# Kernel optimization log

Hardware: AMD Instinct MI355X
Metric: run time of the kernel (lower is better)

## Reference

```python
import jax, jax.numpy as jnp
import numpy as np

SR = 16000
MIN_W = 2.0 * np.pi * 20.0 / SR   # from TimeVaryingLPBiquad(min_w=2*pi*20/sr)
MAX_W = float(np.pi)
MIN_Q = 0.5
MAX_Q = 2.0                        # max_q init arg
MIN_D = 0.1
MAX_D = 2.0

B, T = 32, 65536


def map_logspace(sig, lo, hi):
    # exp-interpolation between lo and hi: lo * (hi/lo)**sig
    return lo * jnp.power(hi / lo, sig)


def setup_inputs() -> dict:
    key = jax.random.key(0)
    k1, k2, k3, k4 = jax.random.split(key, 4)
    f0 = 40.0 + 360.0 * jax.random.uniform(k1, (B, T), dtype=jnp.float32)  # period in samples
    x = jax.random.normal(k2, (B, T), dtype=jnp.float32)
    params = jax.random.normal(k3, (B, T, 4), dtype=jnp.float32)
    onsets = (jax.random.uniform(k4, (B, T)) < 5e-4).astype(jnp.int32)
    return {"f0": f0, "input": x, "params": params, "onsets": onsets}


def _average_per_onset(params, onsets):
    # segment ids = cumulative count of onsets; average params within each segment
    Bb, Tt, C = params.shape
    seg = jnp.cumsum(onsets, axis=1)                       # [B,T] ints in [0, T]
    flat = (jnp.arange(Bb, dtype=seg.dtype)[:, None] * (Tt + 1) + seg).reshape(-1)
    nseg = Bb * (Tt + 1)
    sums = jax.ops.segment_sum(params.reshape(Bb * Tt, C), flat, num_segments=nseg)
    cnt = jax.ops.segment_sum(jnp.ones((Bb * Tt,), params.dtype), flat, num_segments=nseg)
    avg = sums / jnp.maximum(cnt, 1.0)[:, None]
    return avg[flat].reshape(Bb, Tt, C)


def _pluck_comb(f0, mu, x):
    # y[t] = x[t] - (1-alfa)*x[t-(z+1)] - alfa*x[t-(z+2)]  (2 sparse FIR taps)
    Bb, Tt = x.shape
    p = f0 * mu
    z = jnp.floor(p)
    alfa = p - z
    zi = z.astype(jnp.int32)
    t = jnp.arange(Tt, dtype=jnp.int32)[None, :]
    i1 = t - (zi + 1)
    i2 = t - (zi + 2)
    g1 = jnp.take_along_axis(x, jnp.clip(i1, 0, Tt - 1), axis=1)
    g2 = jnp.take_along_axis(x, jnp.clip(i2, 0, Tt - 1), axis=1)
    g1 = jnp.where(i1 >= 0, g1, 0.0)
    g2 = jnp.where(i2 >= 0, g2, 0.0)
    return x - (1.0 - alfa) * g1 - alfa * g2


def _tv_lp_biquad(x, w_mod, q_mod):
    # time-varying RBJ low-pass biquad; cutoff/Q log-interpolated from mods
    w = map_logspace(w_mod, MIN_W, MAX_W)
    q = map_logspace(q_mod, MIN_Q, MAX_Q)
    cw = jnp.cos(w)
    al = jnp.sin(w) / (2.0 * q)
    a0 = 1.0 + al
    b0 = (1.0 - cw) * 0.5 / a0
    b1 = (1.0 - cw) / a0
    b2 = b0
    a1 = (-2.0 * cw) / a0
    a2 = (1.0 - al) / a0

    def step(carry, ct):
        x1, x2, y1, y2 = carry
        cb0, cb1, cb2, ca1, ca2, xn = ct
        y = cb0 * xn + cb1 * x1 + cb2 * x2 - ca1 * y1 - ca2 * y2
        return (xn, x1, y, y1), y

    z = jnp.zeros((x.shape[0],), x.dtype)
    xs = (b0.T, b1.T, b2.T, a1.T, a2.T, x.T)  # time-major [T,B]
    _, ys = jax.lax.scan(step, (z, z, z, z), xs)
    return ys.T


def reference(f0, input, params, onsets):
    p = _average_per_onset(params, onsets)
    distance = map_logspace(jax.nn.sigmoid(p[..., 0]), MIN_D, MAX_D)
    w_mod = jax.nn.sigmoid(p[..., 1])
    q_mod = jax.nn.sigmoid(p[..., 2])
    mu = jax.nn.sigmoid(p[..., 3])
    x = input * distance
    x = _pluck_comb(f0, mu, x)
    y = _tv_lp_biquad(x, w_mod, q_mod)
    return y
```

## Files before the change

kernel.cpp:

```cpp
#include <hip/hip_runtime.h>
#include <math.h>

#define BB 32
#define TT 65536
#define MAXSEG 256
#define CHUNK 8
#define SPB 2048
#define NBLK (BB * TT / SPB)
#define CPR (TT / CHUNK)
#define NCHUNKS (BB * CPR)
#define NGROUPS (NCHUNKS / 64)
#define NSB (BB * TT / 256)
#define HALO 448

#define MIN_W_C 0.007853981633974483f
#define LNW 5.991464547107982f
#define MIN_Q_C 0.5f
#define LNQ 1.3862943611198906f
#define MIN_D_C 0.1f
#define LND 2.995732273553991f

__device__ __forceinline__ int SK(int i)  { return i + (i >> 5); }
__device__ __forceinline__ int SKB(int i) { return i + (i >> 4); }
__device__ __forceinline__ float sigmoidf_(float x) { return 1.0f / (1.0f + expf(-x)); }

__global__ __launch_bounds__(256) void k_count(const int* __restrict__ onsets,
                                               const float* __restrict__ params,
                                               int* __restrict__ bsum,
                                               float4* __restrict__ psum) {
    int tid = threadIdx.x;
    int gid = blockIdx.x * 256 + tid;
    int4 v = ((const int4*)onsets)[gid];
    int c = v.x + v.y + v.z + v.w;
    const float4* pp = ((const float4*)params) + (size_t)gid * 4;
    float4 p0 = pp[0], p1 = pp[1], p2 = pp[2], p3 = pp[3];
    float sx = p0.x + p1.x + p2.x + p3.x;
    float sy = p0.y + p1.y + p2.y + p3.y;
    float sz = p0.z + p1.z + p2.z + p3.z;
    float sw = p0.w + p1.w + p2.w + p3.w;
    for (int off = 32; off; off >>= 1) {
        c  += __shfl_xor(c, off);
        sx += __shfl_xor(sx, off); sy += __shfl_xor(sy, off);
        sz += __shfl_xor(sz, off); sw += __shfl_xor(sw, off);
    }
    if ((tid & 63) == 0) {
        int sb = blockIdx.x * 4 + (tid >> 6);
        bsum[sb] = c;
        psum[sb] = make_float4(sx, sy, sz, sw);
    }
}

__global__ __launch_bounds__(64) void k_rowpre(const int* __restrict__ bsum,
                                               const float4* __restrict__ psum,
                                               int* __restrict__ bpre,
                                               float4* __restrict__ ppre,
                                               float4* __restrict__ rowtot,
                                               int* __restrict__ rown) {
    int r = blockIdx.x, l = threadIdx.x;
    int acc = 0;
    float ax = 0, ay = 0, az = 0, aw = 0;
    for (int g = 0; g < 4; ++g) {
        int sb = r * 256 + g * 64 + l;
        int v = bsum[sb];
        float4 f = psum[sb];
        int x = v;
        float fx = f.x, fy = f.y, fz = f.z, fw = f.w;
        for (int off = 1; off < 64; off <<= 1) {
            int   xy = __shfl_up(x, off);
            float ux = __shfl_up(fx, off), uy = __shfl_up(fy, off);
            float uz = __shfl_up(fz, off), uw = __shfl_up(fw, off);
            if (l >= off) { x += xy; fx += ux; fy += uy; fz += uz; fw += uw; }
        }
        bpre[sb] = acc + x - v;
        ppre[sb] = make_float4(ax + fx - f.x, ay + fy - f.y,
                               az + fz - f.z, aw + fw - f.w);
        acc += __shfl(x, 63);
        ax += __shfl(fx, 63); ay += __shfl(fy, 63);
        az += __shfl(fz, 63); aw += __shfl(fw, 63);
    }
    if (l == 0) { rowtot[r] = make_float4(ax, ay, az, aw); rown[r] = acc; }
}

__global__ __launch_bounds__(256) void k_assign(const int* __restrict__ onsets,
                                                const float* __restrict__ params,
                                                const int* __restrict__ bsum,
                                                const int* __restrict__ bpre,
                                                const float4* __restrict__ ppre,
                                                unsigned char* __restrict__ seg,
                                                int* __restrict__ bndT,
                                                float4* __restrict__ bndP) {
    int blk = blockIdx.x;
    int tid = threadIdx.x;
    int row = blk >> 8;
    size_t g = ((size_t)blk << 8) + tid;
    int bp = bpre[blk];

    if (bsum[blk] == 0) {
        seg[g] = (unsigned char)min(bp, MAXSEG - 1);
        return;
    }

    int on = onsets[g];
    float4 pv = ((const float4*)params)[g];
    int lane = tid & 63, w = tid >> 6;

    int x = on;
    float fx = pv.x, fy = pv.y, fz = pv.z, fw = pv.w;
    for (int off = 1; off < 64; off <<= 1) {
        int   xy = __shfl_up(x, off);
        float ux = __shfl_up(fx, off), uy = __shfl_up(fy, off);
        float uz = __shfl_up(fz, off), uw = __shfl_up(fw, off);
        if (lane >= off) { x += xy; fx += ux; fy += uy; fz += uz; fw += uw; }
    }
    __shared__ int wt[4];
    __shared__ float4 wtf[4];
    if (lane == 63) { wt[w] = x; wtf[w] = make_float4(fx, fy, fz, fw); }
    __syncthreads();
    int wadd = 0;
    float cx = 0, cy = 0, cz = 0, cw = 0;
    for (int i = 0; i < w; ++i) {
        wadd += wt[i];
        float4 t = wtf[i];
        cx += t.x; cy += t.y; cz += t.z; cw += t.w;
    }
    int incl = bp + wadd + x;
    seg[g] = (unsigned char)min(incl, MAXSEG - 1);
    if (on && incl <= MAXSEG - 1) {
        float4 pe = ppre[blk];
        int t_row = ((blk & 255) << 8) + tid;
        bndT[row * 256 + incl] = t_row;
        bndP[row * 256 + incl] = make_float4(pe.x + cx + fx - pv.x,
                                             pe.y + cy + fy - pv.y,
                                             pe.z + cz + fz - pv.z,
                                             pe.w + cw + fw - pv.w);
    }
}

__global__ __launch_bounds__(256) void k_coefs(const int* __restrict__ bndT,
                                               const float4* __restrict__ bndP,
                                               const float4* __restrict__ rowtot,
                                               const int* __restrict__ rown,
                                               float* __restrict__ coef) {
    int s = threadIdx.x, r = blockIdx.x;
    int smax = min(rown[r], MAXSEG - 1);
    int ts; float4 Ps;
    if (s == 0)          { ts = 0;  Ps = make_float4(0, 0, 0, 0); }
    else if (s <= smax)  { ts = bndT[r * 256 + s]; Ps = bndP[r * 256 + s]; }
    else                 { ts = TT; Ps = rowtot[r]; }
    int te; float4 Pe;
    if (s >= smax)       { te = TT; Pe = rowtot[r]; }
    else                 { te = bndT[r * 256 + s + 1]; Pe = bndP[r * 256 + s + 1]; }
    float c = fmaxf((float)(te - ts), 1.0f);
    float p0 = (Pe.x - Ps.x) / c, p1 = (Pe.y - Ps.y) / c;
    float p2 = (Pe.z - Ps.z) / c, p3 = (Pe.w - Ps.w) / c;
    float dist = MIN_D_C * expf(sigmoidf_(p0) * LND);
    float mu   = sigmoidf_(p3);
    float wq   = MIN_W_C * expf(sigmoidf_(p1) * LNW);
    float q    = MIN_Q_C * expf(sigmoidf_(p2) * LNQ);
    float cwv = cosf(wq), sn = sinf(wq);
    float al = sn / (2.0f * q);
    float a0 = 1.0f + al;
    float omc = 1.0f - cwv;
    float b0 = omc * 0.5f / a0;
    float b1 = omc / a0;
    float ca1 = (-2.0f * cwv) / a0;
    float ca2 = (1.0f - al) / a0;
    float4* o = (float4*)(coef + ((size_t)r * 256 + s) * 8);
    o[0] = make_float4(dist, mu, b0, b1);
    o[1] = make_float4(ca1, ca2, 0.0f, 0.0f);
}

__device__ __forceinline__ float comb_pre(const float* __restrict__ in_l,
                                          float f0v, float mu, int lt) {
    float p = f0v * mu;
    int zi = (int)p;
    float alfa = p - (float)zi;
    int i1 = lt - zi - 1;
    float x0 = in_l[SK(HALO + lt)];
    float x1 = in_l[SK(HALO + i1)];
    float x2 = in_l[SK(HALO + i1 - 1)];
    return x0 - (1.0f - alfa) * x1 - alfa * x2;
}

__device__ __forceinline__ void carry_in(const float* __restrict__ in_l,
                                         const unsigned char* __restrict__ seg_l,
                                         const float* __restrict__ f0_l,
                                         const float* __restrict__ f0r,
                                         const float* __restrict__ coefrow,
                                         int base, int t0, float& xm1, float& xm2) {
    xm1 = 0.0f; xm2 = 0.0f;
    int lt = t0 - 1;
    if (base + lt >= 0) {
        int s = seg_l[SKB(HALO + lt)];
        float f0v = (lt >= 0) ? f0_l[SK(lt)] : f0r[base + lt];
        xm1 = comb_pre(in_l, f0v, coefrow[(s << 3) + 1], lt);
    }
    lt = t0 - 2;
    if (base + lt >= 0) {
        int s = seg_l[SKB(HALO + lt)];
        float f0v = (lt >= 0) ? f0_l[SK(lt)] : f0r[base + lt];
        xm2 = comb_pre(in_l, f0v, coefrow[(s << 3) + 1], lt);
    }
}

__device__ __forceinline__ void stage_window(const float* __restrict__ inr,
                                             const float* __restrict__ f0r,
                                             const unsigned char* __restrict__ segr,
                                             const float* __restrict__ coefrow,
                                             int base, int tid,
                                             float* in_l, unsigned char* seg_l,
                                             float* f0_l) {
    for (int i = tid; i < HALO + SPB; i += 256) {
        int g = base - HALO + i;
        unsigned char sv = (g >= 0) ? segr[g] : (unsigned char)0;
        seg_l[SKB(i)] = sv;
        in_l[SK(i)] = (g >= 0) ? inr[g] * coefrow[(int)sv << 3] : 0.0f;
    }
    for (int i = tid; i < SPB; i += 256) f0_l[SK(i)] = f0r[base + i];
}

__global__ __launch_bounds__(256) void k_phase1(const unsigned char* __restrict__ seg,
                                                const float* __restrict__ coef,
                                                const float* __restrict__ f0,
                                                const float* __restrict__ input,
                                                float* __restrict__ AxP,
                                                float* __restrict__ G) {
    __shared__ float in_l[2576];
    __shared__ float f0_l[2112];
    __shared__ unsigned char seg_l[2656];
    const int blk = blockIdx.x, tid = threadIdx.x;
    const int row = blk >> 5;
    const int base = (blk & 31) * SPB;
    const float* inr = input + (size_t)row * TT;
    const float* f0r = f0 + (size_t)row * TT;
    const unsigned char* segr = seg + (size_t)row * TT;
    const float* coefrow = coef + ((size_t)row << 11);

    stage_window(inr, f0r, segr, coefrow, base, tid, in_l, seg_l, f0_l);
    __syncthreads();

    const int t0 = tid * CHUNK;
    float xm1, xm2;
    carry_in(in_l, seg_l, f0_l, f0r, coefrow, base, t0, xm1, xm2);

    int scur = -1;
    float mu = 0, b0 = 0, b1 = 0, ca1 = 0, ca2 = 0;
    float a00 = 1, a01 = 0, a10 = 0, a11 = 1, d0 = 0, d1 = 0;
    #pragma unroll
    for (int j = 0; j < CHUNK; ++j) {
        int lt = t0 + j;
        int s = seg_l[SKB(HALO + lt)];
        if (s != scur) {
            const float4* c4 = (const float4*)(coefrow + (s << 3));
            float4 c0 = c4[0], c1 = c4[1];
            mu = c0.y; b0 = c0.z; b1 = c0.w; ca1 = c1.x; ca2 = c1.y; scur = s;
        }
        float xc = comb_pre(in_l, f0_l[SK(lt)], mu, lt);
        float f = b0 * xc + b1 * xm1 + b0 * xm2;
        xm2 = xm1; xm1 = xc;
        float n00 = -ca1 * a00 - ca2 * a10;
        float n01 = -ca1 * a01 - ca2 * a11;
        float nd0 = f - ca1 * d0 - ca2 * d1;
        a10 = a00; a11 = a01; d1 = d0;
        a00 = n00; a01 = n01; d0 = nd0;
    }
    int lane = tid & 63;
    for (int off = 1; off < 64; off <<= 1) {
        float p00 = __shfl_up(a00, off), p01 = __shfl_up(a01, off);
        float p10 = __shfl_up(a10, off), p11 = __shfl_up(a11, off);
        float pd0 = __shfl_up(d0, off),  pd1 = __shfl_up(d1, off);
        if (lane >= off) {
            float n00 = a00 * p00 + a01 * p10, n01 = a00 * p01 + a01 * p11;
            float n10 = a10 * p00 + a11 * p10, n11 = a10 * p01 + a11 * p11;
            float nd0 = a00 * pd0 + a01 * pd1 + d0, nd1 = a10 * pd0 + a11 * pd1 + d1;
            a00 = n00; a01 = n01; a10 = n10; a11 = n11; d0 = nd0; d1 = nd1;
        }
    }
    int chunkid = blk * 256 + tid;
    AxP[0 * NCHUNKS + chunkid] = a00; AxP[1 * NCHUNKS + chunkid] = a01;
    AxP[2 * NCHUNKS + chunkid] = a10; AxP[3 * NCHUNKS + chunkid] = a11;
    AxP[4 * NCHUNKS + chunkid] = d0;  AxP[5 * NCHUNKS + chunkid] = d1;
    if (lane == 63) {
        int gi = chunkid >> 6;
        G[0 * NGROUPS + gi] = a00; G[1 * NGROUPS + gi] = a01; G[2 * NGROUPS + gi] = a10;
        G[3 * NGROUPS + gi] = a11; G[4 * NGROUPS + gi] = d0;  G[5 * NGROUPS + gi] = d1;
    }
}

__global__ __launch_bounds__(64) void k_scanL2(const float* __restrict__ G,
                                               float* __restrict__ gst0,
                                               float* __restrict__ gst1) {
    int r = blockIdx.x, l = threadIdx.x;
    float c00 = 1, c01 = 0, c10 = 0, c11 = 1, cd0 = 0, cd1 = 0;
    for (int b2 = 0; b2 < 2; ++b2) {
        int gi = r * 128 + b2 * 64 + l;
        float a00 = G[0 * NGROUPS + gi], a01 = G[1 * NGROUPS + gi];
        float a10 = G[2 * NGROUPS + gi], a11 = G[3 * NGROUPS + gi];
        float d0  = G[4 * NGROUPS + gi], d1  = G[5 * NGROUPS + gi];
        for (int off = 1; off < 64; off <<= 1) {
            float p00 = __shfl_up(a00, off), p01 = __shfl_up(a01, off);
            float p10 = __shfl_up(a10, off), p11 = __shfl_up(a11, off);
            float pd0 = __shfl_up(d0, off),  pd1 = __shfl_up(d1, off);
            if (l >= off) {
                float n00 = a00 * p00 + a01 * p10, n01 = a00 * p01 + a01 * p11;
                float n10 = a10 * p00 + a11 * p10, n11 = a10 * p01 + a11 * p11;
                float nd0 = a00 * pd0 + a01 * pd1 + d0, nd1 = a10 * pd0 + a11 * pd1 + d1;
                a00 = n00; a01 = n01; a10 = n10; a11 = n11; d0 = nd0; d1 = nd1;
            }
        }
        float f00 = a00 * c00 + a01 * c10, f01 = a00 * c01 + a01 * c11;
        float f10 = a10 * c00 + a11 * c10, f11 = a10 * c01 + a11 * c11;
        float fd0 = a00 * cd0 + a01 * cd1 + d0, fd1 = a10 * cd0 + a11 * cd1 + d1;
        float e0 = __shfl_up(fd0, 1), e1 = __shfl_up(fd1, 1);
        if (l == 0) { e0 = cd0; e1 = cd1; }
        gst0[gi] = e0; gst1[gi] = e1;
        c00 = __shfl(f00, 63); c01 = __shfl(f01, 63); c10 = __shfl(f10, 63);
        c11 = __shfl(f11, 63); cd0 = __shfl(fd0, 63); cd1 = __shfl(fd1, 63);
    }
}

__global__ __launch_bounds__(256) void k_phase2(const unsigned char* __restrict__ seg,
                                                const float* __restrict__ coef,
                                                const float* __restrict__ f0,
                                                const float* __restrict__ input,
                                                const float* __restrict__ AxP,
                                                const float* __restrict__ gst0,
                                                const float* __restrict__ gst1,
                                                float* __restrict__ out) {
    __shared__ float in_l[2576];
    __shared__ float f0_l[2112];
    __shared__ unsigned char seg_l[2656];
    const int blk = blockIdx.x, tid = threadIdx.x;
    const int row = blk >> 5;
    const int base = (blk & 31) * SPB;
    const float* inr = input + (size_t)row * TT;
    const float* f0r = f0 + (size_t)row * TT;
    const unsigned char* segr = seg + (size_t)row * TT;
    const float* coefrow = coef + ((size_t)row << 11);

    stage_window(inr, f0r, segr, coefrow, base, tid, in_l, seg_l, f0_l);
    __syncthreads();

    const int t0 = tid * CHUNK;
    float xm1, xm2;
    carry_in(in_l, seg_l, f0_l, f0r, coefrow, base, t0, xm1, xm2);
    __syncthreads();

    int chunkid = blk * 256 + tid;
    int lane = tid & 63;
    float g0v = gst0[chunkid >> 6], g1v = gst1[chunkid >> 6];
    float y1, y2;
    if (lane == 0) { y1 = g0v; y2 = g1v; }
    else {
        int q = chunkid - 1;
        float q00 = AxP[0 * NCHUNKS + q], q01 = AxP[1 * NCHUNKS + q];
        float q10 = AxP[2 * NCHUNKS + q], q11 = AxP[3 * NCHUNKS + q];
        float qd0 = AxP[4 * NCHUNKS + q], qd1 = AxP[5 * NCHUNKS + q];
        y1 = q00 * g0v + q01 * g1v + qd0;
        y2 = q10 * g0v + q11 * g1v + qd1;
    }

    int scur = -1;
    float mu = 0, b0 = 0, b1 = 0, ca1 = 0, ca2 = 0;
    #pragma unroll
    for (int j = 0; j < CHUNK; ++j) {
        int lt = t0 + j;
        int s = seg_l[SKB(HALO + lt)];
        if (s != scur) {
            const float4* c4 = (const float4*)(coefrow + (s << 3));
            float4 c0 = c4[0], c1 = c4[1];
            mu = c0.y; b0 = c0.z; b1 = c0.w; ca1 = c1.x; ca2 = c1.y; scur = s;
        }
        float xc = comb_pre(in_l, f0_l[SK(lt)], mu, lt);
        float f = b0 * xc + b1 * xm1 + b0 * xm2;
        xm2 = xm1; xm1 = xc;
        float y = f - ca1 * y1 - ca2 * y2;
        y2 = y1; y1 = y;
        f0_l[SK(lt)] = y;
    }
    __syncthreads();
    float* outr = out + (size_t)row * TT + base;
    for (int i = tid; i < SPB; i += 256) outr[i] = f0_l[SK(i)];
}

extern "C" void kernel_launch(void* const* d_in, const int* in_sizes, int n_in,
                              void* d_out, int out_size, void* d_ws, size_t ws_size,
                              hipStream_t stream) {
    const float* f0     = (const float*)d_in[0];
    const float* input  = (const float*)d_in[1];
    const float* params = (const float*)d_in[2];
    const int*   onsets = (const int*)d_in[3];
    float* out = (float*)d_out;

    char* ws = (char*)d_ws;
    int*           bsum   = (int*)   (ws + 0);
    int*           bpre   = (int*)   (ws + 32768);
    float4*        psum   = (float4*)(ws + 65536);
    float4*        ppre   = (float4*)(ws + 196608);
    float4*        rowtot = (float4*)(ws + 327680);
    int*           rown   = (int*)   (ws + 328192);
    int*           bndT   = (int*)   (ws + 328320);
    float4*        bndP   = (float4*)(ws + 361088);
    float*         coef   = (float*) (ws + 492160);
    unsigned char* seg    = (unsigned char*)(ws + 754304);
    float*         AxP    = (float*) (ws + 2851456);
    float*         G      = (float*) (ws + 9142912);
    float*         gst0   = (float*) (ws + 9241216);
    float*         gst1   = (float*) (ws + 9257600);

    k_count <<<2048, 256, 0, stream>>>(onsets, params, bsum, psum);
    k_rowpre<<<BB, 64, 0, stream>>>(bsum, psum, bpre, ppre, rowtot, rown);
    k_assign<<<NSB, 256, 0, stream>>>(onsets, params, bsum, bpre, ppre, seg, bndT, bndP);
    k_coefs <<<BB, 256, 0, stream>>>(bndT, bndP, rowtot, rown, coef);
    k_phase1<<<NBLK, 256, 0, stream>>>(seg, coef, f0, input, AxP, G);
    k_scanL2<<<BB, 64, 0, stream>>>(G, gst0, gst1);
    k_phase2<<<NBLK, 256, 0, stream>>>(seg, coef, f0, input, AxP, gst0, gst1, out);
}
```

Baseline: 133.8 us.

## Fuse coef and L2 scan kernels into phases, store FIR output for phase2

Removes the k_coefs and k_scanL2 launches: each phase block recomputes per-segment biquad coefficients into shared memory, and phase2 redoes the per-row group scan redundantly per wave. Phase1 now writes the feed-forward comb+FIR output to a global buffer, so phase2 only runs the recursive part and no longer restages input, f0 and the halo or recomputes the comb. f0 and output are moved with vectorized float4 accesses in registers. This trades two fewer launches and less phase2 work for an extra 8 MB global write/read and redundant transcendental math per block.

```diff
diff --git a/kernel.cpp b/kernel.cpp
--- a/kernel.cpp
+++ b/kernel.cpp
@@ -7,8 +7,7 @@
 #define CHUNK 8
 #define SPB 2048
 #define NBLK (BB * TT / SPB)
-#define CPR (TT / CHUNK)
-#define NCHUNKS (BB * CPR)
+#define NCHUNKS (BB * TT / CHUNK)
 #define NGROUPS (NCHUNKS / 64)
 #define NSB (BB * TT / 256)
 #define HALO 448
@@ -23,6 +22,53 @@
 __device__ __forceinline__ int SK(int i)  { return i + (i >> 5); }
 __device__ __forceinline__ int SKB(int i) { return i + (i >> 4); }
 __device__ __forceinline__ float sigmoidf_(float x) { return 1.0f / (1.0f + expf(-x)); }
+
+__device__ __forceinline__ void wscan6(int lane, float& a00, float& a01, float& a10,
+                                       float& a11, float& d0, float& d1) {
+    for (int off = 1; off < 64; off <<= 1) {
+        float p00 = __shfl_up(a00, off), p01 = __shfl_up(a01, off);
+        float p10 = __shfl_up(a10, off), p11 = __shfl_up(a11, off);
+        float pd0 = __shfl_up(d0, off),  pd1 = __shfl_up(d1, off);
+        if (lane >= off) {
+            float n00 = a00 * p00 + a01 * p10, n01 = a00 * p01 + a01 * p11;
+            float n10 = a10 * p00 + a11 * p10, n11 = a10 * p01 + a11 * p11;
+            float nd0 = a00 * pd0 + a01 * pd1 + d0, nd1 = a10 * pd0 + a11 * pd1 + d1;
+            a00 = n00; a01 = n01; a10 = n10; a11 = n11; d0 = nd0; d1 = nd1;
+        }
+    }
+}
+
+__device__ __forceinline__ void seg_coefs(int s, int row,
+                                          const int* __restrict__ bndT,
+                                          const float4* __restrict__ bndP,
+                                          const float4* __restrict__ rowtot,
+                                          const int* __restrict__ rown,
+                                          float& dist, float& mu, float& b0, float& b1,
+                                          float& ca1, float& ca2) {
+    int smax = min(rown[row], MAXSEG - 1);
+    int ts; float4 Ps;
+    if (s == 0)         { ts = 0;  Ps = make_float4(0, 0, 0, 0); }
+    else if (s <= smax) { ts = bndT[row * 256 + s]; Ps = bndP[row * 256 + s]; }
+    else                { ts = TT; Ps = rowtot[row]; }
+    int te; float4 Pe;
+    if (s >= smax)      { te = TT; Pe = rowtot[row]; }
+    else                { te = bndT[row * 256 + s + 1]; Pe = bndP[row * 256 + s + 1]; }
+    float c = fmaxf((float)(te - ts), 1.0f);
+    float p0 = (Pe.x - Ps.x) / c, p1 = (Pe.y - Ps.y) / c;
+    float p2 = (Pe.z - Ps.z) / c, p3 = (Pe.w - Ps.w) / c;
+    dist = MIN_D_C * expf(sigmoidf_(p0) * LND);
+    mu   = sigmoidf_(p3);
+    float wq = MIN_W_C * expf(sigmoidf_(p1) * LNW);
+    float q  = MIN_Q_C * expf(sigmoidf_(p2) * LNQ);
+    float cwv = cosf(wq), sn = sinf(wq);
+    float al = sn / (2.0f * q);
+    float a0 = 1.0f + al;
+    float omc = 1.0f - cwv;
+    b0 = omc * 0.5f / a0;
+    b1 = omc / a0;
+    ca1 = (-2.0f * cwv) / a0;
+    ca2 = (1.0f - al) / a0;
+}
 
 __global__ __launch_bounds__(256) void k_count(const int* __restrict__ onsets,
                                                const float* __restrict__ params,
@@ -136,40 +182,6 @@
     }
 }
 
-__global__ __launch_bounds__(256) void k_coefs(const int* __restrict__ bndT,
-                                               const float4* __restrict__ bndP,
-                                               const float4* __restrict__ rowtot,
-                                               const int* __restrict__ rown,
-                                               float* __restrict__ coef) {
-    int s = threadIdx.x, r = blockIdx.x;
-    int smax = min(rown[r], MAXSEG - 1);
-    int ts; float4 Ps;
-    if (s == 0)          { ts = 0;  Ps = make_float4(0, 0, 0, 0); }
-    else if (s <= smax)  { ts = bndT[r * 256 + s]; Ps = bndP[r * 256 + s]; }
-    else                 { ts = TT; Ps = rowtot[r]; }
-    int te; float4 Pe;
-    if (s >= smax)       { te = TT; Pe = rowtot[r]; }
-    else                 { te = bndT[r * 256 + s + 1]; Pe = bndP[r * 256 + s + 1]; }
-    float c = fmaxf((float)(te - ts), 1.0f);
-    float p0 = (Pe.x - Ps.x) / c, p1 = (Pe.y - Ps.y) / c;
-    float p2 = (Pe.z - Ps.z) / c, p3 = (Pe.w - Ps.w) / c;
-    float dist = MIN_D_C * expf(sigmoidf_(p0) * LND);
-    float mu   = sigmoidf_(p3);
-    float wq   = MIN_W_C * expf(sigmoidf_(p1) * LNW);
-    float q    = MIN_Q_C * expf(sigmoidf_(p2) * LNQ);
-    float cwv = cosf(wq), sn = sinf(wq);
-    float al = sn / (2.0f * q);
-    float a0 = 1.0f + al;
-    float omc = 1.0f - cwv;
-    float b0 = omc * 0.5f / a0;
-    float b1 = omc / a0;
-    float ca1 = (-2.0f * cwv) / a0;
-    float ca2 = (1.0f - al) / a0;
-    float4* o = (float4*)(coef + ((size_t)r * 256 + s) * 8);
-    o[0] = make_float4(dist, mu, b0, b1);
-    o[1] = make_float4(ca1, ca2, 0.0f, 0.0f);
-}
-
 __device__ __forceinline__ float comb_pre(const float* __restrict__ in_l,
                                           float f0v, float mu, int lt) {
     float p = f0v * mu;
@@ -182,100 +194,100 @@
     return x0 - (1.0f - alfa) * x1 - alfa * x2;
 }
 
-__device__ __forceinline__ void carry_in(const float* __restrict__ in_l,
-                                         const unsigned char* __restrict__ seg_l,
-                                         const float* __restrict__ f0_l,
-                                         const float* __restrict__ f0r,
-                                         const float* __restrict__ coefrow,
-                                         int base, int t0, float& xm1, float& xm2) {
-    xm1 = 0.0f; xm2 = 0.0f;
-    int lt = t0 - 1;
-    if (base + lt >= 0) {
-        int s = seg_l[SKB(HALO + lt)];
-        float f0v = (lt >= 0) ? f0_l[SK(lt)] : f0r[base + lt];
-        xm1 = comb_pre(in_l, f0v, coefrow[(s << 3) + 1], lt);
-    }
-    lt = t0 - 2;
-    if (base + lt >= 0) {
-        int s = seg_l[SKB(HALO + lt)];
-        float f0v = (lt >= 0) ? f0_l[SK(lt)] : f0r[base + lt];
-        xm2 = comb_pre(in_l, f0v, coefrow[(s << 3) + 1], lt);
-    }
-}
-
-__device__ __forceinline__ void stage_window(const float* __restrict__ inr,
-                                             const float* __restrict__ f0r,
-                                             const unsigned char* __restrict__ segr,
-                                             const float* __restrict__ coefrow,
-                                             int base, int tid,
-                                             float* in_l, unsigned char* seg_l,
-                                             float* f0_l) {
-    for (int i = tid; i < HALO + SPB; i += 256) {
-        int g = base - HALO + i;
-        unsigned char sv = (g >= 0) ? segr[g] : (unsigned char)0;
-        seg_l[SKB(i)] = sv;
-        in_l[SK(i)] = (g >= 0) ? inr[g] * coefrow[(int)sv << 3] : 0.0f;
-    }
-    for (int i = tid; i < SPB; i += 256) f0_l[SK(i)] = f0r[base + i];
-}
-
 __global__ __launch_bounds__(256) void k_phase1(const unsigned char* __restrict__ seg,
-                                                const float* __restrict__ coef,
+                                                const int* __restrict__ bndT,
+                                                const float4* __restrict__ bndP,
+                                                const float4* __restrict__ rowtot,
+                                                const int* __restrict__ rown,
                                                 const float* __restrict__ f0,
                                                 const float* __restrict__ input,
+                                                float* __restrict__ fglob,
                                                 float* __restrict__ AxP,
                                                 float* __restrict__ G) {
     __shared__ float in_l[2576];
-    __shared__ float f0_l[2112];
     __shared__ unsigned char seg_l[2656];
+    __shared__ float4 coefA[256];
+    __shared__ float2 coefB[256];
     const int blk = blockIdx.x, tid = threadIdx.x;
     const int row = blk >> 5;
     const int base = (blk & 31) * SPB;
+    const int wstart = base - HALO;
     const float* inr = input + (size_t)row * TT;
     const float* f0r = f0 + (size_t)row * TT;
     const unsigned char* segr = seg + (size_t)row * TT;
-    const float* coefrow = coef + ((size_t)row << 11);
-
-    stage_window(inr, f0r, segr, coefrow, base, tid, in_l, seg_l, f0_l);
+
+    {
+        float dist, mu, b0, b1, ca1, ca2;
+        seg_coefs(tid, row, bndT, bndP, rowtot, rown, dist, mu, b0, b1, ca1, ca2);
+        coefA[tid] = make_float4(dist, mu, b0, b1);
+        coefB[tid] = make_float2(ca1, ca2);
+    }
+    for (int i = tid; i < HALO + SPB; i += 256) {
+        int g = wstart + i;
+        seg_l[SKB(i)] = (g >= 0) ? segr[g] : (unsigned char)0;
+    }
     __syncthreads();
+    for (int q = tid; q < (HALO + SPB) / 4; q += 256) {
+        int g4 = wstart + q * 4;
+        float4 v = (g4 >= 0) ? *(const float4*)(inr + g4) : make_float4(0, 0, 0, 0);
+        in_l[SK(q * 4 + 0)] = v.x * coefA[seg_l[SKB(q * 4 + 0)]].x;
+        in_l[SK(q * 4 + 1)] = v.y * coefA[seg_l[SKB(q * 4 + 1)]].x;
+        in_l[SK(q * 4 + 2)] = v.z * coefA[seg_l[SKB(q * 4 + 2)]].x;
+        in_l[SK(q * 4 + 3)] = v.w * coefA[seg_l[SKB(q * 4 + 3)]].x;
+    }
+    __syncthreads();
 
     const int t0 = tid * CHUNK;
-    float xm1, xm2;
-    carry_in(in_l, seg_l, f0_l, f0r, coefrow, base, t0, xm1, xm2);
+    float f0v[8];
+    {
+        const float4* f4 = (const float4*)(f0r + base);
+        float4 A = f4[tid * 2], B = f4[tid * 2 + 1];
+        f0v[0] = A.x; f0v[1] = A.y; f0v[2] = A.z; f0v[3] = A.w;
+        f0v[4] = B.x; f0v[5] = B.y; f0v[6] = B.z; f0v[7] = B.w;
+    }
+    float xm1 = 0.0f, xm2 = 0.0f;
+    {
+        int lt = t0 - 1;
+        if (base + lt >= 0) {
+            int s = seg_l[SKB(HALO + lt)];
+            xm1 = comb_pre(in_l, f0r[base + lt], coefA[s].y, lt);
+        }
+        lt = t0 - 2;
+        if (base + lt >= 0) {
+            int s = seg_l[SKB(HALO + lt)];
+            xm2 = comb_pre(in_l, f0r[base + lt], coefA[s].y, lt);
+        }
+    }
 
     int scur = -1;
     float mu = 0, b0 = 0, b1 = 0, ca1 = 0, ca2 = 0;
     float a00 = 1, a01 = 0, a10 = 0, a11 = 1, d0 = 0, d1 = 0;
+    float fv[8];
     #pragma unroll
     for (int j = 0; j < CHUNK; ++j) {
         int lt = t0 + j;
         int s = seg_l[SKB(HALO + lt)];
         if (s != scur) {
-            const float4* c4 = (const float4*)(coefrow + (s << 3));
-            float4 c0 = c4[0], c1 = c4[1];
-            mu = c0.y; b0 = c0.z; b1 = c0.w; ca1 = c1.x; ca2 = c1.y; scur = s;
+            float4 cA = coefA[s]; float2 cB = coefB[s];
+            mu = cA.y; b0 = cA.z; b1 = cA.w; ca1 = cB.x; ca2 = cB.y; scur = s;
         }
-        float xc = comb_pre(in_l, f0_l[SK(lt)], mu, lt);
+        float xc = comb_pre(in_l, f0v[j], mu, lt);
         float f = b0 * xc + b1 * xm1 + b0 * xm2;
         xm2 = xm1; xm1 = xc;
+        fv[j] = f;
         float n00 = -ca1 * a00 - ca2 * a10;
         float n01 = -ca1 * a01 - ca2 * a11;
         float nd0 = f - ca1 * d0 - ca2 * d1;
         a10 = a00; a11 = a01; d1 = d0;
         a00 = n00; a01 = n01; d0 = nd0;
     }
+    {
+        float4* fr4 = (float4*)(fglob + (size_t)row * TT + base);
+        fr4[tid * 2]     = make_float4(fv[0], fv[1], fv[2], fv[3]);
+        fr4[tid * 2 + 1] = make_float4(fv[4], fv[5], fv[6], fv[7]);
+    }
     int lane = tid & 63;
-    for (int off = 1; off < 64; off <<= 1) {
-        float p00 = __shfl_up(a00, off), p01 = __shfl_up(a01, off);
-        float p10 = __shfl_up(a10, off), p11 = __shfl_up(a11, off);
-        float pd0 = __shfl_up(d0, off),  pd1 = __shfl_up(d1, off);
-        if (lane >= off) {
-            float n00 = a00 * p00 + a01 * p10, n01 = a00 * p01 + a01 * p11;
-            float n10 = a10 * p00 + a11 * p10, n11 = a10 * p01 + a11 * p11;
-            float nd0 = a00 * pd0 + a01 * pd1 + d0, nd1 = a10 * pd0 + a11 * pd1 + d1;
-            a00 = n00; a01 = n01; a10 = n10; a11 = n11; d0 = nd0; d1 = nd1;
-        }
-    }
+    wscan6(lane, a00, a01, a10, a11, d0, d1);
     int chunkid = blk * 256 + tid;
     AxP[0 * NCHUNKS + chunkid] = a00; AxP[1 * NCHUNKS + chunkid] = a01;
     AxP[2 * NCHUNKS + chunkid] = a10; AxP[3 * NCHUNKS + chunkid] = a11;
@@ -287,100 +299,88 @@
     }
 }
 
-__global__ __launch_bounds__(64) void k_scanL2(const float* __restrict__ G,
-                                               float* __restrict__ gst0,
-                                               float* __restrict__ gst1) {
-    int r = blockIdx.x, l = threadIdx.x;
-    float c00 = 1, c01 = 0, c10 = 0, c11 = 1, cd0 = 0, cd1 = 0;
-    for (int b2 = 0; b2 < 2; ++b2) {
-        int gi = r * 128 + b2 * 64 + l;
-        float a00 = G[0 * NGROUPS + gi], a01 = G[1 * NGROUPS + gi];
-        float a10 = G[2 * NGROUPS + gi], a11 = G[3 * NGROUPS + gi];
-        float d0  = G[4 * NGROUPS + gi], d1  = G[5 * NGROUPS + gi];
-        for (int off = 1; off < 64; off <<= 1) {
-            float p00 = __shfl_up(a00, off), p01 = __shfl_up(a01, off);
-            float p10 = __shfl_up(a10, off), p11 = __shfl_up(a11, off);
-            float pd0 = __shfl_up(d0, off),  pd1 = __shfl_up(d1, off);
-            if (l >= off) {
-                float n00 = a00 * p00 + a01 * p10, n01 = a00 * p01 + a01 * p11;
-                float n10 = a10 * p00 + a11 * p10, n11 = a10 * p01 + a11 * p11;
-                float nd0 = a00 * pd0 + a01 * pd1 + d0, nd1 = a10 * pd0 + a11 * pd1 + d1;
-                a00 = n00; a01 = n01; a10 = n10; a11 = n11; d0 = nd0; d1 = nd1;
-            }
-        }
-        float f00 = a00 * c00 + a01 * c10, f01 = a00 * c01 + a01 * c11;
-        float f10 = a10 * c00 + a11 * c10, f11 = a10 * c01 + a11 * c11;
-        float fd0 = a00 * cd0 + a01 * cd1 + d0, fd1 = a10 * cd0 + a11 * cd1 + d1;
-        float e0 = __shfl_up(fd0, 1), e1 = __shfl_up(fd1, 1);
-        if (l == 0) { e0 = cd0; e1 = cd1; }
-        gst0[gi] = e0; gst1[gi] = e1;
-        c00 = __shfl(f00, 63); c01 = __shfl(f01, 63); c10 = __shfl(f10, 63);
-        c11 = __shfl(f11, 63); cd0 = __shfl(fd0, 63); cd1 = __shfl(fd1, 63);
-    }
-}
-
 __global__ __launch_bounds__(256) void k_phase2(const unsigned char* __restrict__ seg,
-                                                const float* __restrict__ coef,
-                                                const float* __restrict__ f0,
-                                                const float* __restrict__ input,
+                                                const int* __restrict__ bndT,
+                                                const float4* __restrict__ bndP,
+                                                const float4* __restrict__ rowtot,
+                                                const int* __restrict__ rown,
+                                                const float* __restrict__ fglob,
                                                 const float* __restrict__ AxP,
-                                                const float* __restrict__ gst0,
-                                                const float* __restrict__ gst1,
+                                                const float* __restrict__ G,
                                                 float* __restrict__ out) {
-    __shared__ float in_l[2576];
-    __shared__ float f0_l[2112];
-    __shared__ unsigned char seg_l[2656];
+    __shared__ float2 ca_l[256];
     const int blk = blockIdx.x, tid = threadIdx.x;
     const int row = blk >> 5;
     const int base = (blk & 31) * SPB;
-    const float* inr = input + (size_t)row * TT;
-    const float* f0r = f0 + (size_t)row * TT;
-    const unsigned char* segr = seg + (size_t)row * TT;
-    const float* coefrow = coef + ((size_t)row << 11);
-
-    stage_window(inr, f0r, segr, coefrow, base, tid, in_l, seg_l, f0_l);
+
+    {
+        float dist, mu, b0, b1, ca1, ca2;
+        seg_coefs(tid, row, bndT, bndP, rowtot, rown, dist, mu, b0, b1, ca1, ca2);
+        ca_l[tid] = make_float2(ca1, ca2);
+    }
     __syncthreads();
 
     const int t0 = tid * CHUNK;
-    float xm1, xm2;
-    carry_in(in_l, seg_l, f0_l, f0r, coefrow, base, t0, xm1, xm2);
-    __syncthreads();
+    float fv[8];
+    {
+        const float4* f4 = (const float4*)(fglob + (size_t)row * TT + base);
+        float4 A = f4[tid * 2], B = f4[tid * 2 + 1];
+        fv[0] = A.x; fv[1] = A.y; fv[2] = A.z; fv[3] = A.w;
+        fv[4] = B.x; fv[5] = B.y; fv[6] = B.z; fv[7] = B.w;
+    }
+    uint2 sv = *(const uint2*)(seg + (size_t)row * TT + base + t0);
+
+    int lane = tid & 63, wv = tid >> 6;
+    int gown = (blk & 31) * 4 + wv;
+    int gb = row * 128;
+    float a00 = G[0 * NGROUPS + gb + lane], a01 = G[1 * NGROUPS + gb + lane];
+    float a10 = G[2 * NGROUPS + gb + lane], a11 = G[3 * NGROUPS + gb + lane];
+    float d0  = G[4 * NGROUPS + gb + lane], d1  = G[5 * NGROUPS + gb + lane];
+    wscan6(lane, a00, a01, a10, a11, d0, d1);
+    float r0d0 = d0, r0d1 = d1;
+    float c00 = __shfl(a00, 63), c01 = __shfl(a01, 63);
+    float c10 = __shfl(a10, 63), c11 = __shfl(a11, 63);
+    float cd0 = __shfl(d0, 63),  cd1 = __shfl(d1, 63);
+    float e0, e1;
+    if (gown == 0) { e0 = 0.0f; e1 = 0.0f; }
+    else if (gown <= 64) {
+        e0 = __shfl(r0d0, gown - 1); e1 = __shfl(r0d1, gown - 1);
+    } else {
+        float b00 = G[0 * NGROUPS + gb + 64 + lane], b01 = G[1 * NGROUPS + gb + 64 + lane];
+        float b10 = G[2 * NGROUPS + gb + 64 + lane], b11 = G[3 * NGROUPS + gb + 64 + lane];
+        float e0v = G[4 * NGROUPS + gb + 64 + lane], e1v = G[5 * NGROUPS + gb + 64 + lane];
+        wscan6(lane, b00, b01, b10, b11, e0v, e1v);
+        float fd0 = b00 * cd0 + b01 * cd1 + e0v;
+        float fd1 = b10 * cd0 + b11 * cd1 + e1v;
+        e0 = __shfl(fd0, gown - 65); e1 = __shfl(fd1, gown - 65);
+    }
 
     int chunkid = blk * 256 + tid;
-    int lane = tid & 63;
-    float g0v = gst0[chunkid >> 6], g1v = gst1[chunkid >> 6];
     float y1, y2;
-    if (lane == 0) { y1 = g0v; y2 = g1v; }
+    if (lane == 0) { y1 = e0; y2 = e1; }
     else {
         int q = chunkid - 1;
         float q00 = AxP[0 * NCHUNKS + q], q01 = AxP[1 * NCHUNKS + q];
         float q10 = AxP[2 * NCHUNKS + q], q11 = AxP[3 * NCHUNKS + q];
         float qd0 = AxP[4 * NCHUNKS + q], qd1 = AxP[5 * NCHUNKS + q];
-        y1 = q00 * g0v + q01 * g1v + qd0;
-        y2 = q10 * g0v + q11 * g1v + qd1;
+        y1 = q00 * e0 + q01 * e1 + qd0;
+        y2 = q10 * e0 + q11 * e1 + qd1;
     }
 
     int scur = -1;
-    float mu = 0, b0 = 0, b1 = 0, ca1 = 0, ca2 = 0;
+    float ca1 = 0, ca2 = 0;
+    float ov[8];
     #pragma unroll
     for (int j = 0; j < CHUNK; ++j) {
-        int lt = t0 + j;
-        int s = seg_l[SKB(HALO + lt)];
-        if (s != scur) {
-            const float4* c4 = (const float4*)(coefrow + (s << 3));
-            float4 c0 = c4[0], c1 = c4[1];
-            mu = c0.y; b0 = c0.z; b1 = c0.w; ca1 = c1.x; ca2 = c1.y; scur = s;
-        }
-        float xc = comb_pre(in_l, f0_l[SK(lt)], mu, lt);
-        float f = b0 * xc + b1 * xm1 + b0 * xm2;
-        xm2 = xm1; xm1 = xc;
-        float y = f - ca1 * y1 - ca2 * y2;
+        int s = (int)((j < 4 ? (sv.x >> (8 * j)) : (sv.y >> (8 * (j - 4)))) & 255u);
+        if (s != scur) { float2 c = ca_l[s]; ca1 = c.x; ca2 = c.y; scur = s; }
+        float y = fv[j] - ca1 * y1 - ca2 * y2;
         y2 = y1; y1 = y;
-        f0_l[SK(lt)] = y;
-    }
-    __syncthreads();
-    float* outr = out + (size_t)row * TT + base;
-    for (int i = tid; i < SPB; i += 256) outr[i] = f0_l[SK(i)];
+        ov[j] = y;
+    }
+    float4* o4 = (float4*)(out + (size_t)row * TT + base);
+    o4[tid * 2]     = make_float4(ov[0], ov[1], ov[2], ov[3]);
+    o4[tid * 2 + 1] = make_float4(ov[4], ov[5], ov[6], ov[7]);
 }
 
 extern "C" void kernel_launch(void* const* d_in, const int* in_sizes, int n_in,
@@ -401,18 +401,15 @@
     int*           rown   = (int*)   (ws + 328192);
     int*           bndT   = (int*)   (ws + 328320);
     float4*        bndP   = (float4*)(ws + 361088);
-    float*         coef   = (float*) (ws + 492160);
-    unsigned char* seg    = (unsigned char*)(ws + 754304);
-    float*         AxP    = (float*) (ws + 2851456);
-    float*         G      = (float*) (ws + 9142912);
-    float*         gst0   = (float*) (ws + 9241216);
-    float*         gst1   = (float*) (ws + 9257600);
+    unsigned char* seg    = (unsigned char*)(ws + 492160);
+    float*         AxP    = (float*) (ws + 2589312);
+    float*         G      = (float*) (ws + 8880768);
+    float*         fglob  = (float*) (ws + 8979072);
 
     k_count <<<2048, 256, 0, stream>>>(onsets, params, bsum, psum);
     k_rowpre<<<BB, 64, 0, stream>>>(bsum, psum, bpre, ppre, rowtot, rown);
     k_assign<<<NSB, 256, 0, stream>>>(onsets, params, bsum, bpre, ppre, seg, bndT, bndP);
-    k_coefs <<<BB, 256, 0, stream>>>(bndT, bndP, rowtot, rown, coef);
-    k_phase1<<<NBLK, 256, 0, stream>>>(seg, coef, f0, input, AxP, G);
-    k_scanL2<<<BB, 64, 0, stream>>>(G, gst0, gst1);
-    k_phase2<<<NBLK, 256, 0, stream>>>(seg, coef, f0, input, AxP, gst0, gst1, out);
-}
+    k_phase1<<<NBLK, 256, 0, stream>>>(seg, bndT, bndP, rowtot, rown, f0, input,
+                                       fglob, AxP, G);
+    k_phase2<<<NBLK, 256, 0, stream>>>(seg, bndT, bndP, rowtot, rown, fglob, AxP, G, out);
+}
```

After: 124.1 us. 1.08x faster.
